# Optimization experiments

Hardware: AMD Instinct MI355X
Metric: run time of the kernel (lower is better)

Reference implementation:

```python
import jax, jax.numpy as jnp
import numpy as np

B, S, D, H = 2, 4096, 768, 12
HD = D // H  # head_dim = 64


def setup_inputs() -> dict:
    key = jax.random.key(0)
    ks = jax.random.split(key, 12)
    s = 0.02
    inp = {
        'q': jax.random.normal(ks[0], (B, S, D), jnp.float32),
        'k': jax.random.normal(ks[1], (B, S, D), jnp.float32),
        'v': jax.random.normal(ks[2], (B, S, D), jnp.float32),
        # True = masked position (filled with -inf); causal mask, broadcastable
        'mask': jnp.triu(jnp.ones((S, S), jnp.bool_), k=1)[None, None],
        'Wq': jax.random.normal(ks[3], (D, D), jnp.float32) * s,
        'bq': jnp.zeros((D,), jnp.float32),
        'Wk': jax.random.normal(ks[4], (D, D), jnp.float32) * s,
        'bk': jnp.zeros((D,), jnp.float32),
        'Wv': jax.random.normal(ks[5], (D, D), jnp.float32) * s,
        'bv': jnp.zeros((D,), jnp.float32),
        'Wo': jax.random.normal(ks[6], (D, D), jnp.float32) * s,
        'bo': jnp.zeros((D,), jnp.float32),
    }
    return inp


def _split_heads(x):
    # [B, S, D] -> [B, H, S, HD]
    return x.reshape(B, S, H, HD).transpose(0, 2, 1, 3)


def reference(q, k, v, mask, Wq, bq, Wk, bk, Wv, bv, Wo, bo):
    # per-head linear projections (torch Linear: x @ W.T + b)
    qh = _split_heads(q @ Wq.T + bq)
    kh = _split_heads(k @ Wk.T + bk)
    vh = _split_heads(v @ Wv.T + bv)
    scale = 1.0 / np.sqrt(HD).astype(np.float32)
    # naive full [B, H, S, S] attention scores (module materializes these)
    wei = jnp.einsum('bhqd,bhkd->bhqk', qh, kh) * scale
    wei = jnp.where(mask, -jnp.inf, wei)
    attn = jax.nn.softmax(wei, axis=-1)
    feats = jnp.einsum('bhqk,bhkd->bhqd', attn, vh)
    # concat heads: [B, H, S, HD] -> [B, S, D]
    out = feats.transpose(0, 2, 1, 3).reshape(B, S, D)
    return out @ Wo.T + bo
```

## Files before the change

### kernel.cpp

```cpp
#include <hip/hip_runtime.h>
#include <math.h>

#define B_  2
#define S_  4096
#define D_  768
#define H_  12
#define HD_ 64

using bf16x8  = __attribute__((ext_vector_type(8))) __bf16;
using f32x4   = __attribute__((ext_vector_type(4))) float;
using ushort8 = __attribute__((ext_vector_type(8))) unsigned short;
using uintv2  = __attribute__((ext_vector_type(2))) unsigned;
using uintv4  = __attribute__((ext_vector_type(4))) unsigned;

__device__ __forceinline__ unsigned short f2b(float f) {
    union { float f; unsigned u; } x; x.f = f;
    unsigned r = x.u + 0x7fffu + ((x.u >> 16) & 1u);
    return (unsigned short)(r >> 16);
}
__device__ __forceinline__ unsigned pk2(float x, float y) {
    unsigned ux = __builtin_bit_cast(unsigned, x) + 0x8000u;
    unsigned uy = __builtin_bit_cast(unsigned, y) + 0x8000u;
    return (uy & 0xFFFF0000u) | (ux >> 16);
}
__device__ __forceinline__ unsigned cvtpk(float lo, float hi) {
    unsigned r;
    asm("v_cvt_pk_bf16_f32 %0, %1, %2" : "=v"(r) : "v"(lo), "v"(hi));
    return r;
}
__device__ __forceinline__ uintv2 xpose_pair(unsigned x, unsigned y) {
    uintv2 s = __builtin_amdgcn_permlane32_swap(x, y, false, false);
    return __builtin_amdgcn_permlane16_swap(s[0], s[1], false, false);
}

__global__ __launch_bounds__(256)
void w_convert(const float* __restrict__ Wq, const float* __restrict__ Wk,
               const float* __restrict__ Wv, const float* __restrict__ Wo,
               unsigned short* __restrict__ Wb)
{
    const int z = blockIdx.y;
    const float* src = (z == 0) ? Wq : (z == 1) ? Wk : (z == 2) ? Wv : Wo;
    unsigned short* dst = Wb + (size_t)z * (D_ * D_);
    int idx = blockIdx.x * 256 + threadIdx.x;
    const float4 a = *(const float4*)(src + (size_t)idx * 8);
    const float4 b = *(const float4*)(src + (size_t)idx * 8 + 4);
    uint4 o;
    o.x = pk2(a.x, a.y); o.y = pk2(a.z, a.w);
    o.z = pk2(b.x, b.y); o.w = pk2(b.z, b.w);
    *(uint4*)(dst + (size_t)idx * 8) = o;
}

__global__ __launch_bounds__(256)
void qkv_gemm(const float* __restrict__ q, const float* __restrict__ k,
              const float* __restrict__ v,
              const unsigned short* __restrict__ Wb,
              const float* __restrict__ bq, const float* __restrict__ bk,
              const float* __restrict__ bv,
              unsigned short* __restrict__ Qp, unsigned short* __restrict__ Kp,
              unsigned short* __restrict__ Vrm)
{
    constexpr int BM = 128, BN = 128, BK = 32, LDP = 40;
    const int z = blockIdx.z;
    const float* A    = (z == 0) ? q  : (z == 1) ? k  : v;
    const unsigned short* W = Wb + (size_t)z * (D_ * D_);
    const float* bias = (z == 0) ? bq : (z == 1) ? bk : bv;
    unsigned short* C = (z == 0) ? Qp : (z == 1) ? Kp : Vrm;

    __shared__ __align__(16) unsigned short As[BM * LDP];
    __shared__ __align__(16) unsigned short Bs[BN * LDP];

    const int tid = threadIdx.x, bm = blockIdx.x, bn = blockIdx.y;
    const int w = tid >> 6, lane = tid & 63, lr = lane & 15, lg = lane >> 4;
    const int wm = (w >> 1) * 64, wn = (w & 1) * 64;

    f32x4 acc[4][4] = {};

    for (int k0 = 0; k0 < D_; k0 += BK) {
        __syncthreads();
        for (int t = 0; t < 4; ++t) {
            int idx = tid + t * 256, row = idx >> 3, c4 = (idx & 7) * 4;
            float4 va = *(const float4*)(A + (size_t)(bm * BM + row) * D_ + k0 + c4);
            *(uint2*)&As[row * LDP + c4] = make_uint2(pk2(va.x, va.y), pk2(va.z, va.w));
        }
        for (int t = 0; t < 2; ++t) {
            int idx = tid + t * 256, row = idx >> 2, c8 = (idx & 3) * 8;
            *(ushort8*)&Bs[row * LDP + c8] =
                *(const ushort8*)(W + (size_t)(bn * BN + row) * D_ + k0 + c8);
        }
        __syncthreads();
        bf16x8 af[4], bfr[4];
        for (int i = 0; i < 4; ++i) af[i]  = *(const bf16x8*)&As[(wm + i * 16 + lr) * LDP + lg * 8];
        for (int j = 0; j < 4; ++j) bfr[j] = *(const bf16x8*)&Bs[(wn + j * 16 + lr) * LDP + lg * 8];
        for (int i = 0; i < 4; ++i)
            for (int j = 0; j < 4; ++j)
                acc[i][j] = __builtin_amdgcn_mfma_f32_16x16x32_bf16(af[i], bfr[j], acc[i][j], 0, 0, 0);
    }

    const float qscale = 0.18033688011112042f;
    for (int i = 0; i < 4; ++i) {
        int row0 = bm * BM + wm + i * 16 + lg * 4;
        for (int j = 0; j < 4; ++j) {
            int col = bn * BN + wn + j * 16 + lr;
            float bv_ = bias[col];
            for (int r = 0; r < 4; ++r) {
                float val = acc[i][j][r] + bv_;
                if (z == 0) val *= qscale;
                C[(size_t)(row0 + r) * D_ + col] = f2b(val);
            }
        }
    }
}

__global__ __launch_bounds__(256)
void v_transpose(const unsigned short* __restrict__ Vrm,
                 unsigned short* __restrict__ Vt)
{
    __shared__ __align__(16) unsigned short T[64][72];
    const int st = blockIdx.x, bh = blockIdx.y;
    const int b = bh / H_, h = bh % H_;
    const int tid = threadIdx.x;

    for (int t = 0; t < 2; ++t) {
        int idx = tid + t * 256, s = idx >> 3, c8 = (idx & 7) * 8;
        *(ushort8*)&T[s][c8] =
            *(const ushort8*)(Vrm + ((size_t)(b * S_ + st * 64 + s)) * D_ + h * HD_ + c8);
    }
    __syncthreads();
    const int d = tid >> 2;
    for (int it = 0; it < 2; ++it) {
        int s8 = (tid & 3) + it * 4;
        ushort8 val;
        for (int j = 0; j < 8; ++j) val[j] = T[s8 * 8 + j][d];
        *(ushort8*)(Vt + ((size_t)bh * HD_ + d) * S_ + st * 64 + s8 * 8) = val;
    }
}

__global__ __launch_bounds__(256)
void o_gemm(const unsigned short* __restrict__ Ai, const unsigned short* __restrict__ W,
            const float* __restrict__ bias, float* __restrict__ C)
{
    constexpr int BM = 128, BN = 64, BK = 32, LDP = 40;
    __shared__ __align__(16) unsigned short As[BM * LDP];
    __shared__ __align__(16) unsigned short Bs[BN * LDP];

    const int tid = threadIdx.x, bm = blockIdx.x, bn = blockIdx.y;
    const int w = tid >> 6, lane = tid & 63, lr = lane & 15, lg = lane >> 4;
    const int wm = (w >> 1) * 64, wn = (w & 1) * 32;

    f32x4 acc[4][2] = {};

    for (int k0 = 0; k0 < D_; k0 += BK) {
        __syncthreads();
        for (int t = 0; t < 2; ++t) {
            int idx = tid + t * 256, row = idx >> 2, c8 = (idx & 3) * 8;
            *(ushort8*)&As[row * LDP + c8] =
                *(const ushort8*)(Ai + (size_t)(bm * BM + row) * D_ + k0 + c8);
        }
        {
            int row = tid >> 2, c8 = (tid & 3) * 8;
            *(ushort8*)&Bs[row * LDP + c8] =
                *(const ushort8*)(W + (size_t)(bn * BN + row) * D_ + k0 + c8);
        }
        __syncthreads();
        bf16x8 af[4], bfr[2];
        for (int i = 0; i < 4; ++i) af[i]  = *(const bf16x8*)&As[(wm + i * 16 + lr) * LDP + lg * 8];
        for (int j = 0; j < 2; ++j) bfr[j] = *(const bf16x8*)&Bs[(wn + j * 16 + lr) * LDP + lg * 8];
        for (int i = 0; i < 4; ++i)
            for (int j = 0; j < 2; ++j)
                acc[i][j] = __builtin_amdgcn_mfma_f32_16x16x32_bf16(af[i], bfr[j], acc[i][j], 0, 0, 0);
    }

    for (int i = 0; i < 4; ++i) {
        int row0 = bm * BM + wm + i * 16 + lg * 4;
        for (int j = 0; j < 2; ++j) {
            int col = bn * BN + wn + j * 16 + lr;
            float bv_ = bias[col];
            for (int r = 0; r < 4; ++r)
                C[(size_t)(row0 + r) * D_ + col] = acc[i][j][r] + bv_;
        }
    }
}

__global__ __launch_bounds__(256)
void attn_kernel(const unsigned short* __restrict__ Qp,
                 const unsigned short* __restrict__ Kp,
                 const unsigned short* __restrict__ Vt,
                 unsigned short* __restrict__ feats)
{
    __shared__ __align__(16) unsigned short Ks[2][64 * 72];
    __shared__ __align__(16) unsigned short Vs[2][64 * 72];

    const int tid = threadIdx.x;
    const int lin = blockIdx.x + gridDim.x * blockIdx.y;
    const int xcd = lin & 7, idx = lin >> 3;
    const int bh  = xcd * 3 + (idx >> 5);
    const int p   = idx & 31;
    const int b = bh / H_, h = bh % H_;
    const int w = tid >> 6, lane = tid & 63, lr = lane & 15, lg = lane >> 4;

    const int qtA = 63 - p, qtB = p;

    bf16x8 ones;
    for (int j = 0; j < 8; ++j) ones[j] = (__bf16)1.0f;

    const size_t kbase = ((size_t)b * S_) * D_ + h * HD_;
    const size_t vbase = ((size_t)bh * HD_) * S_;

    const size_t qbA = ((size_t)(b * S_ + qtA * 64 + w * 16 + lr)) * D_ + h * HD_;
    const size_t qbB = ((size_t)(b * S_ + qtB * 64 + w * 16 + lr)) * D_ + h * HD_;
    bf16x8 qfA0 = *(const bf16x8*)(Qp + qbA + lg * 8);
    bf16x8 qfA1 = *(const bf16x8*)(Qp + qbA + 32 + lg * 8);
    bf16x8 qfB0 = *(const bf16x8*)(Qp + qbB + lg * 8);
    bf16x8 qfB1 = *(const bf16x8*)(Qp + qbB + 32 + lg * 8);

    f32x4 oA[4] = {}, oB[4] = {};
    f32x4 lA = {0.f, 0.f, 0.f, 0.f}, lB = {0.f, 0.f, 0.f, 0.f};

    const int nst = qtA + 1;

    const int srow = tid >> 3, sc8 = (tid & 7) * 8;
    const unsigned short* kpt = Kp + kbase + (size_t)srow * D_ + sc8;
    const unsigned short* vpt = Vt + vbase + (size_t)srow * S_ + sc8;
    unsigned short* KsW0 = &Ks[0][srow * 72 + sc8];
    unsigned short* VsW0 = &Vs[0][srow * 72 + sc8];
    unsigned short* KsW1 = &Ks[1][srow * 72 + sc8];
    unsigned short* VsW1 = &Vs[1][srow * 72 + sc8];

    {
        ushort8 a0 = *(const ushort8*)(kpt);
        ushort8 a1 = *(const ushort8*)(kpt + (size_t)32 * D_);
        ushort8 a2 = *(const ushort8*)(vpt);
        ushort8 a3 = *(const ushort8*)(vpt + (size_t)32 * S_);
        *(ushort8*)KsW0            = a0;
        *(ushort8*)(KsW0 + 32*72)  = a1;
        *(ushort8*)VsW0            = a2;
        *(ushort8*)(VsW0 + 32*72)  = a3;
    }
    __syncthreads();

    for (int kb = 0; kb < nst; ++kb) {
        const bool bAct = (kb <= qtB);
        const int cur = kb & 1;
        const unsigned short* Kc = Ks[cur];
        const unsigned short* Vc = Vs[cur];

        const int kb2 = (kb + 1 < nst) ? kb + 1 : kb;
        const unsigned short* kp2 = kpt + (size_t)kb2 * 64 * D_;
        const unsigned short* vp2 = vpt + (size_t)kb2 * 64;
        ushort8 kr0 = *(const ushort8*)(kp2);
        ushort8 kr1 = *(const ushort8*)(kp2 + (size_t)32 * D_);
        ushort8 vr0 = *(const ushort8*)(vp2);
        ushort8 vr1 = *(const ushort8*)(vp2 + (size_t)32 * S_);

        bf16x8 kf[4][2];
        for (int n = 0; n < 4; ++n) {
            kf[n][0] = *(const bf16x8*)&Kc[(n * 16 + lr) * 72 + lg * 8];
            kf[n][1] = *(const bf16x8*)&Kc[(n * 16 + lr) * 72 + 32 + lg * 8];
        }

        bf16x8 pfA0, pfA1, pfB0, pfB1;

        {
            f32x4 st[4];
            for (int n = 0; n < 4; ++n) {
                f32x4 s = {0.f, 0.f, 0.f, 0.f};
                s = __builtin_amdgcn_mfma_f32_16x16x32_bf16(kf[n][0], qfA0, s, 0, 0, 0);
                s = __builtin_amdgcn_mfma_f32_16x16x32_bf16(kf[n][1], qfA1, s, 0, 0, 0);
                st[n] = s;
            }
            if (kb == qtA) {
                for (int n = 0; n < 4; ++n)
                    for (int r = 0; r < 4; ++r)
                        if (n * 16 + lg * 4 + r > w * 16 + lr) st[n][r] = -INFINITY;
            }
            unsigned a_[4][2];
            for (int n = 0; n < 4; ++n) {
                float e0 = __builtin_amdgcn_exp2f(st[n][0]);
                float e1 = __builtin_amdgcn_exp2f(st[n][1]);
                float e2 = __builtin_amdgcn_exp2f(st[n][2]);
                float e3 = __builtin_amdgcn_exp2f(st[n][3]);
                a_[n][0] = cvtpk(e0, e1);
                a_[n][1] = cvtpk(e2, e3);
            }
            uintv2 p00 = xpose_pair(a_[0][0], a_[1][0]);
            uintv2 p01 = xpose_pair(a_[0][1], a_[1][1]);
            uintv2 p10 = xpose_pair(a_[2][0], a_[3][0]);
            uintv2 p11 = xpose_pair(a_[2][1], a_[3][1]);
            uintv4 w0 = {p00[0], p01[0], p00[1], p01[1]};
            uintv4 w1 = {p10[0], p11[0], p10[1], p11[1]};
            pfA0 = __builtin_bit_cast(bf16x8, w0);
            pfA1 = __builtin_bit_cast(bf16x8, w1);
        }
        if (bAct) {
            f32x4 st[4];
            for (int n = 0; n < 4; ++n) {
                f32x4 s = {0.f, 0.f, 0.f, 0.f};
                s = __builtin_amdgcn_mfma_f32_16x16x32_bf16(kf[n][0], qfB0, s, 0, 0, 0);
                s = __builtin_amdgcn_mfma_f32_16x16x32_bf16(kf[n][1], qfB1, s, 0, 0, 0);
                st[n] = s;
            }
            if (kb == qtB) {
                for (int n = 0; n < 4; ++n)
                    for (int r = 0; r < 4; ++r)
                        if (n * 16 + lg * 4 + r > w * 16 + lr) st[n][r] = -INFINITY;
            }
            unsigned a_[4][2];
            for (int n = 0; n < 4; ++n) {
                float e0 = __builtin_amdgcn_exp2f(st[n][0]);
                float e1 = __builtin_amdgcn_exp2f(st[n][1]);
                float e2 = __builtin_amdgcn_exp2f(st[n][2]);
                float e3 = __builtin_amdgcn_exp2f(st[n][3]);
                a_[n][0] = cvtpk(e0, e1);
                a_[n][1] = cvtpk(e2, e3);
            }
            uintv2 p00 = xpose_pair(a_[0][0], a_[1][0]);
            uintv2 p01 = xpose_pair(a_[0][1], a_[1][1]);
            uintv2 p10 = xpose_pair(a_[2][0], a_[3][0]);
            uintv2 p11 = xpose_pair(a_[2][1], a_[3][1]);
            uintv4 w0 = {p00[0], p01[0], p00[1], p01[1]};
            uintv4 w1 = {p10[0], p11[0], p10[1], p11[1]};
            pfB0 = __builtin_bit_cast(bf16x8, w0);
            pfB1 = __builtin_bit_cast(bf16x8, w1);
        }

        bf16x8 vf[4][2];
        for (int n = 0; n < 4; ++n) {
            vf[n][0] = *(const bf16x8*)&Vc[(n * 16 + lr) * 72 + lg * 8];
            vf[n][1] = *(const bf16x8*)&Vc[(n * 16 + lr) * 72 + 32 + lg * 8];
        }
        {
            for (int n = 0; n < 4; ++n) {
                oA[n] = __builtin_amdgcn_mfma_f32_16x16x32_bf16(vf[n][0], pfA0, oA[n], 0, 0, 0);
                oA[n] = __builtin_amdgcn_mfma_f32_16x16x32_bf16(vf[n][1], pfA1, oA[n], 0, 0, 0);
            }
            lA = __builtin_amdgcn_mfma_f32_16x16x32_bf16(ones, pfA0, lA, 0, 0, 0);
            lA = __builtin_amdgcn_mfma_f32_16x16x32_bf16(ones, pfA1, lA, 0, 0, 0);
        }
        if (bAct) {
            for (int n = 0; n < 4; ++n) {
                oB[n] = __builtin_amdgcn_mfma_f32_16x16x32_bf16(vf[n][0], pfB0, oB[n], 0, 0, 0);
                oB[n] = __builtin_amdgcn_mfma_f32_16x16x32_bf16(vf[n][1], pfB1, oB[n], 0, 0, 0);
            }
            lB = __builtin_amdgcn_mfma_f32_16x16x32_bf16(ones, pfB0, lB, 0, 0, 0);
            lB = __builtin_amdgcn_mfma_f32_16x16x32_bf16(ones, pfB1, lB, 0, 0, 0);
        }

        if (cur == 0) {
            *(ushort8*)KsW1            = kr0;
            *(ushort8*)(KsW1 + 32*72)  = kr1;
            *(ushort8*)VsW1            = vr0;
            *(ushort8*)(VsW1 + 32*72)  = vr1;
        } else {
            *(ushort8*)KsW0            = kr0;
            *(ushort8*)(KsW0 + 32*72)  = kr1;
            *(ushort8*)VsW0            = vr0;
            *(ushort8*)(VsW0 + 32*72)  = vr1;
        }
        __syncthreads();
    }

    {
        const float inv = 1.0f / lA[0];
        const size_t obase = ((size_t)(b * S_ + qtA * 64 + w * 16 + lr)) * D_ + h * HD_;
        for (int n = 0; n < 4; ++n) {
            unsigned short e0 = f2b(oA[n][0] * inv), e1 = f2b(oA[n][1] * inv);
            unsigned short e2 = f2b(oA[n][2] * inv), e3 = f2b(oA[n][3] * inv);
            *(uint2*)(feats + obase + n * 16 + lg * 4) =
                make_uint2((unsigned)e0 | ((unsigned)e1 << 16),
                           (unsigned)e2 | ((unsigned)e3 << 16));
        }
    }
    {
        const float inv = 1.0f / lB[0];
        const size_t obase = ((size_t)(b * S_ + qtB * 64 + w * 16 + lr)) * D_ + h * HD_;
        for (int n = 0; n < 4; ++n) {
            unsigned short e0 = f2b(oB[n][0] * inv), e1 = f2b(oB[n][1] * inv);
            unsigned short e2 = f2b(oB[n][2] * inv), e3 = f2b(oB[n][3] * inv);
            *(uint2*)(feats + obase + n * 16 + lg * 4) =
                make_uint2((unsigned)e0 | ((unsigned)e1 << 16),
                           (unsigned)e2 | ((unsigned)e3 << 16));
        }
    }
}

extern "C" void kernel_launch(void* const* d_in, const int* in_sizes, int n_in,
                              void* d_out, int out_size, void* d_ws, size_t ws_size,
                              hipStream_t stream) {
    const float* q  = (const float*)d_in[0];
    const float* k  = (const float*)d_in[1];
    const float* v  = (const float*)d_in[2];
    const float* Wq = (const float*)d_in[4];
    const float* bq = (const float*)d_in[5];
    const float* Wk = (const float*)d_in[6];
    const float* bk = (const float*)d_in[7];
    const float* Wv = (const float*)d_in[8];
    const float* bv = (const float*)d_in[9];
    const float* Wo = (const float*)d_in[10];
    const float* bo = (const float*)d_in[11];
    float* out = (float*)d_out;

    const size_t npro = (size_t)B_ * S_ * D_;
    const size_t nw   = (size_t)D_ * D_;
    unsigned short* Qp    = (unsigned short*)d_ws;
    unsigned short* Kp    = Qp + npro;
    unsigned short* Vrm   = Kp + npro;
    unsigned short* Vt    = Vrm + npro;
    unsigned short* Wb    = Vt + npro;
    unsigned short* feats = Vrm;

    dim3 blk(256);
    w_convert<<<dim3(288, 4), blk, 0, stream>>>(Wq, Wk, Wv, Wo, Wb);
    qkv_gemm<<<dim3(64, 6, 3), blk, 0, stream>>>(q, k, v, Wb, bq, bk, bv,
                                                 Qp, Kp, Vrm);
    v_transpose<<<dim3(S_ / 64, B_ * H_), blk, 0, stream>>>(Vrm, Vt);
    attn_kernel<<<dim3(32, B_ * H_), blk, 0, stream>>>(Qp, Kp, Vt, feats);
    o_gemm<<<dim3(64, 12), blk, 0, stream>>>(feats, Wb + 3 * nw, bo, out);
}
```

Before: 333.7 us.

## Double-buffer QKV and output GEMM tiles; reorder attention block-to-work mapping

Both projection GEMMs now keep two shared-memory tile buffers and register-prefetch the next K slice from global memory while MFMAs run on the current one. This cuts the loop to one barrier per iteration and hides global load latency. The attention kernel also permutes the pair index p differently for each of the three heads a given XCD handles, so causal workloads are spread more evenly across blocks scheduled at the same time. The costs are doubled LDS use in the GEMMs, which may reduce occupancy, and more registers held live for the prefetched data.

```diff
diff --git a/kernel.cpp b/kernel.cpp
--- a/kernel.cpp
+++ b/kernel.cpp
@@ -59,41 +59,58 @@
               unsigned short* __restrict__ Qp, unsigned short* __restrict__ Kp,
               unsigned short* __restrict__ Vrm)
 {
-    constexpr int BM = 128, BN = 128, BK = 32, LDP = 40;
+    constexpr int BM = 128, BN = 128, BK = 32, LDP = 40, NK = D_ / BK;
     const int z = blockIdx.z;
     const float* A    = (z == 0) ? q  : (z == 1) ? k  : v;
     const unsigned short* W = Wb + (size_t)z * (D_ * D_);
     const float* bias = (z == 0) ? bq : (z == 1) ? bk : bv;
     unsigned short* C = (z == 0) ? Qp : (z == 1) ? Kp : Vrm;
 
-    __shared__ __align__(16) unsigned short As[BM * LDP];
-    __shared__ __align__(16) unsigned short Bs[BN * LDP];
+    __shared__ __align__(16) unsigned short As[2][BM * LDP];
+    __shared__ __align__(16) unsigned short Bs[2][BN * LDP];
 
     const int tid = threadIdx.x, bm = blockIdx.x, bn = blockIdx.y;
     const int w = tid >> 6, lane = tid & 63, lr = lane & 15, lg = lane >> 4;
     const int wm = (w >> 1) * 64, wn = (w & 1) * 64;
 
+    const int arow = tid >> 3, ac4 = (tid & 7) * 4;
+    const int brow = tid >> 2, bc8 = (tid & 3) * 8;
+    const float* Abase = A + (size_t)(bm * BM + arow) * D_ + ac4;
+    const unsigned short* Wbase = W + (size_t)(bn * BN + brow) * D_ + bc8;
+
+    float4 ap[4]; ushort8 bp[2];
+
+    for (int t = 0; t < 4; ++t) ap[t] = *(const float4*)(Abase + (size_t)t * 32 * D_);
+    for (int t = 0; t < 2; ++t) bp[t] = *(const ushort8*)(Wbase + (size_t)t * 64 * D_);
+    for (int t = 0; t < 4; ++t)
+        *(uint2*)&As[0][(arow + t * 32) * LDP + ac4] =
+            make_uint2(pk2(ap[t].x, ap[t].y), pk2(ap[t].z, ap[t].w));
+    for (int t = 0; t < 2; ++t)
+        *(ushort8*)&Bs[0][(brow + t * 64) * LDP + bc8] = bp[t];
+    __syncthreads();
+
     f32x4 acc[4][4] = {};
 
-    for (int k0 = 0; k0 < D_; k0 += BK) {
-        __syncthreads();
-        for (int t = 0; t < 4; ++t) {
-            int idx = tid + t * 256, row = idx >> 3, c4 = (idx & 7) * 4;
-            float4 va = *(const float4*)(A + (size_t)(bm * BM + row) * D_ + k0 + c4);
-            *(uint2*)&As[row * LDP + c4] = make_uint2(pk2(va.x, va.y), pk2(va.z, va.w));
-        }
-        for (int t = 0; t < 2; ++t) {
-            int idx = tid + t * 256, row = idx >> 2, c8 = (idx & 3) * 8;
-            *(ushort8*)&Bs[row * LDP + c8] =
-                *(const ushort8*)(W + (size_t)(bn * BN + row) * D_ + k0 + c8);
-        }
-        __syncthreads();
+    for (int it = 0; it < NK; ++it) {
+        const int cur = it & 1;
+        const int k2 = ((it + 1 < NK) ? it + 1 : it) * BK;
+        for (int t = 0; t < 4; ++t) ap[t] = *(const float4*)(Abase + k2 + (size_t)t * 32 * D_);
+        for (int t = 0; t < 2; ++t) bp[t] = *(const ushort8*)(Wbase + k2 + (size_t)t * 64 * D_);
+
         bf16x8 af[4], bfr[4];
-        for (int i = 0; i < 4; ++i) af[i]  = *(const bf16x8*)&As[(wm + i * 16 + lr) * LDP + lg * 8];
-        for (int j = 0; j < 4; ++j) bfr[j] = *(const bf16x8*)&Bs[(wn + j * 16 + lr) * LDP + lg * 8];
+        for (int i = 0; i < 4; ++i) af[i]  = *(const bf16x8*)&As[cur][(wm + i * 16 + lr) * LDP + lg * 8];
+        for (int j = 0; j < 4; ++j) bfr[j] = *(const bf16x8*)&Bs[cur][(wn + j * 16 + lr) * LDP + lg * 8];
         for (int i = 0; i < 4; ++i)
             for (int j = 0; j < 4; ++j)
                 acc[i][j] = __builtin_amdgcn_mfma_f32_16x16x32_bf16(af[i], bfr[j], acc[i][j], 0, 0, 0);
+
+        const int nxt = cur ^ 1;
+        for (int t = 0; t < 4; ++t)
+            *(uint2*)&As[nxt][(arow + t * 32) * LDP + ac4] =
+                make_uint2(pk2(ap[t].x, ap[t].y), pk2(ap[t].z, ap[t].w));
+        for (int t = 0; t < 2; ++t)
+            *(ushort8*)&Bs[nxt][(brow + t * 64) * LDP + bc8] = bp[t];
+        __syncthreads();
     }
 
     const float qscale = 0.18033688011112042f;
@@ -139,35 +156,46 @@
 void o_gemm(const unsigned short* __restrict__ Ai, const unsigned short* __restrict__ W,
             const float* __restrict__ bias, float* __restrict__ C)
 {
-    constexpr int BM = 128, BN = 64, BK = 32, LDP = 40;
-    __shared__ __align__(16) unsigned short As[BM * LDP];
-    __shared__ __align__(16) unsigned short Bs[BN * LDP];
+    constexpr int BM = 128, BN = 64, BK = 32, LDP = 40, NK = D_ / BK;
+    __shared__ __align__(16) unsigned short As[2][BM * LDP];
+    __shared__ __align__(16) unsigned short Bs[2][BN * LDP];
 
     const int tid = threadIdx.x, bm = blockIdx.x, bn = blockIdx.y;
     const int w = tid >> 6, lane = tid & 63, lr = lane & 15, lg = lane >> 4;
     const int wm = (w >> 1) * 64, wn = (w & 1) * 32;
 
+    const int arow = tid >> 2, ac8 = (tid & 3) * 8;
+    const unsigned short* Abase = Ai + (size_t)(bm * BM + arow) * D_ + ac8;
+    const unsigned short* Wbase = W + (size_t)(bn * BN + arow) * D_ + ac8;
+
+    ushort8 apre[2], bpre;
+    for (int t = 0; t < 2; ++t) apre[t] = *(const ushort8*)(Abase + (size_t)t * 64 * D_);
+    bpre = *(const ushort8*)(Wbase);
+    for (int t = 0; t < 2; ++t)
+        *(ushort8*)&As[0][(arow + t * 64) * LDP + ac8] = apre[t];
+    *(ushort8*)&Bs[0][arow * LDP + ac8] = bpre;
+    __syncthreads();
+
     f32x4 acc[4][2] = {};
 
-    for (int k0 = 0; k0 < D_; k0 += BK) {
-        __syncthreads();
-        for (int t = 0; t < 2; ++t) {
-            int idx = tid + t * 256, row = idx >> 2, c8 = (idx & 3) * 8;
-            *(ushort8*)&As[row * LDP + c8] =
-                *(const ushort8*)(Ai + (size_t)(bm * BM + row) * D_ + k0 + c8);
-        }
-        {
-            int row = tid >> 2, c8 = (tid & 3) * 8;
-            *(ushort8*)&Bs[row * LDP + c8] =
-                *(const ushort8*)(W + (size_t)(bn * BN + row) * D_ + k0 + c8);
-        }
-        __syncthreads();
+    for (int it = 0; it < NK; ++it) {
+        const int cur = it & 1;
+        const int k2 = ((it + 1 < NK) ? it + 1 : it) * BK;
+        for (int t = 0; t < 2; ++t) apre[t] = *(const ushort8*)(Abase + k2 + (size_t)t * 64 * D_);
+        bpre = *(const ushort8*)(Wbase + k2);
+
         bf16x8 af[4], bfr[2];
-        for (int i = 0; i < 4; ++i) af[i]  = *(const bf16x8*)&As[(wm + i * 16 + lr) * LDP + lg * 8];
-        for (int j = 0; j < 2; ++j) bfr[j] = *(const bf16x8*)&Bs[(wn + j * 16 + lr) * LDP + lg * 8];
+        for (int i = 0; i < 4; ++i) af[i]  = *(const bf16x8*)&As[cur][(wm + i * 16 + lr) * LDP + lg * 8];
+        for (int j = 0; j < 2; ++j) bfr[j] = *(const bf16x8*)&Bs[cur][(wn + j * 16 + lr) * LDP + lg * 8];
         for (int i = 0; i < 4; ++i)
             for (int j = 0; j < 2; ++j)
                 acc[i][j] = __builtin_amdgcn_mfma_f32_16x16x32_bf16(af[i], bfr[j], acc[i][j], 0, 0, 0);
+
+        const int nxt = cur ^ 1;
+        for (int t = 0; t < 2; ++t)
+            *(ushort8*)&As[nxt][(arow + t * 64) * LDP + ac8] = apre[t];
+        *(ushort8*)&Bs[nxt][arow * LDP + ac8] = bpre;
+        __syncthreads();
     }
 
     for (int i = 0; i < 4; ++i) {
@@ -193,8 +221,13 @@
     const int tid = threadIdx.x;
     const int lin = blockIdx.x + gridDim.x * blockIdx.y;
     const int xcd = lin & 7, idx = lin >> 3;
-    const int bh  = xcd * 3 + (idx >> 5);
-    const int p   = idx & 31;
+    const int bhl = idx >> 5;
+    const int i   = idx & 31;
+    int p;
+    if (bhl == 0)      p = i;
+    else if (bhl == 1) p = (i + 16) & 31;
+    else               p = (i < 16) ? (31 - 2 * i) : (62 - 2 * i);
+    const int bh  = xcd * 3 + bhl;
     const int b = bh / H_, h = bh % H_;
     const int w = tid >> 6, lane = tid & 63, lr = lane & 15, lg = lane >> 4;
 
```

Measured after the change: 325.9 us. -2.3%, faster.
